# Optimization experiments

Hardware: AMD Instinct MI355X
Metric: run time of the kernel (lower is better)

## Reference

```python
import jax, jax.numpy as jnp
import numpy as np

B, L, HID = 32, 1, 3072
H, KV, D = 16, 8, 256
S = 2048
SCALE = D ** -0.5


def setup_inputs() -> dict:
    key = jax.random.key(0)
    ks = jax.random.split(key, 10)
    return {
        "hidden_states": jax.random.normal(ks[0], (B, L, HID), jnp.float32),
        "freqs_cos": jax.random.normal(ks[1], (B, L, D // 2), jnp.float32),
        "freqs_sin": jax.random.normal(ks[2], (B, L, D // 2), jnp.float32),
        "mask": jnp.zeros((B, 1, 1, S), jnp.float32),
        "cache_k": jax.random.normal(ks[3], (B, KV, S, D), jnp.float32),
        "cache_v": jax.random.normal(ks[4], (B, KV, S, D), jnp.float32),
        "wq": jax.random.normal(ks[5], (HID, H * D), jnp.float32) * 0.02,
        "wk": jax.random.normal(ks[6], (HID, KV * D), jnp.float32) * 0.02,
        "wv": jax.random.normal(ks[7], (HID, KV * D), jnp.float32) * 0.02,
        "wo": jax.random.normal(ks[8], (H * D, HID), jnp.float32) * 0.02,
        "pos": 2047,
    }


def _rope(x, cos, sin):
    # x: [B, L, nh, D]; cos/sin: [B, L, D/2]. Split-half complex rotation:
    # pairs are (x[..., i], x[..., i + D/2]), matching torch chunk+view_as_complex.
    half = x.shape[-1] // 2
    xr, xi = x[..., :half], x[..., half:]
    c = cos[:, :, None, :]
    s = sin[:, :, None, :]
    return jnp.concatenate([xr * c - xi * s, xr * s + xi * c], axis=-1)


def reference(hidden_states, freqs_cos, freqs_sin, mask, cache_k, cache_v,
              wq, wk, wv, wo, pos):
    G = H // KV  # queries per kv head
    xq = (hidden_states @ wq).reshape(B, L, H, D)
    xk = (hidden_states @ wk).reshape(B, L, KV, D)
    xv = (hidden_states @ wv).reshape(B, L, KV, D)

    xq = _rope(xq, freqs_cos, freqs_sin)
    xk = _rope(xk, freqs_cos, freqs_sin)

    # [B, heads, L, D]
    xq = xq.transpose(0, 2, 1, 3)
    xk = xk.transpose(0, 2, 1, 3)
    xv = xv.transpose(0, 2, 1, 3)

    # insert current step into the KV cache at static position `pos`
    cache_k = cache_k.at[:, :, pos:pos + L, :].set(xk)
    cache_v = cache_v.at[:, :, pos:pos + L, :].set(xv)

    # GQA attention over the full cache without materializing repeated KV
    q = xq.reshape(B, KV, G, L, D)
    scores = jnp.einsum('bkgqd,bksd->bkgqs', q, cache_k) * SCALE
    scores = scores + mask[:, :, None]  # [B,1,1,1,S] broadcast
    probs = jax.nn.softmax(scores, axis=-1)
    out = jnp.einsum('bkgqs,bksd->bkgqd', probs, cache_v)

    out = out.reshape(B, H, L, D).transpose(0, 2, 1, 3).reshape(B, L, H * D)
    return out @ wo
```

## Files before the change

### kernel.cpp

```cpp
#include <hip/hip_runtime.h>
#include <hip/hip_bf16.h>


#define SCALE_ 0.0625f

#define OFF_XQKV (8u*32u*8192u)
#define OFF_ATTN (OFF_XQKV + 32u*8192u)
#define OFF_PO   (OFF_ATTN + 32u*4096u)
#define OFF_ML   (1048576u)

__device__ inline void fma4(float4& a, float s, const float4& w) {
  a.x = fmaf(s, w.x, a.x); a.y = fmaf(s, w.y, a.y);
  a.z = fmaf(s, w.z, a.z); a.w = fmaf(s, w.w, a.w);
}
__device__ inline float dot4(const float4& a, const float4& b) {
  return a.x * b.x + a.y * b.y + a.z * b.z + a.w * b.w;
}
__device__ inline void scale_fma4(float4& a, float sc, float p, const float4& v) {
  a.x = fmaf(a.x, sc, p * v.x); a.y = fmaf(a.y, sc, p * v.y);
  a.z = fmaf(a.z, sc, p * v.z); a.w = fmaf(a.w, sc, p * v.w);
}

__global__ __launch_bounds__(512) void qkv_partial_kernel(
    const float* __restrict__ x, const float* __restrict__ wq,
    const float* __restrict__ wk, const float* __restrict__ wv,
    float* __restrict__ pqkv) {
  const int lane = threadIdx.x & 63;
  const int bg   = threadIdx.x >> 6;
  const int ctile = blockIdx.x & 31;
  const int kc    = blockIdx.x >> 5;
  const int n = ctile * 256 + lane * 4;

  const float* w; int stride, nn;
  if (n < 4096)      { w = wq; stride = 4096; nn = n; }
  else if (n < 6144) { w = wk; stride = 2048; nn = n - 4096; }
  else               { w = wv; stride = 2048; nn = n - 6144; }

  const float* wb = w + (size_t)(kc * 384) * stride + nn;
  const float* xb = x + (size_t)(bg * 4) * 3072 + kc * 384;

  float4 acc[4];
#pragma unroll
  for (int j = 0; j < 4; ++j) acc[j] = make_float4(0.f, 0.f, 0.f, 0.f);

  for (int k = 0; k < 384; k += 4) {
    float4 w0 = *(const float4*)(wb + (size_t)(k + 0) * stride);
    float4 w1 = *(const float4*)(wb + (size_t)(k + 1) * stride);
    float4 w2 = *(const float4*)(wb + (size_t)(k + 2) * stride);
    float4 w3 = *(const float4*)(wb + (size_t)(k + 3) * stride);
#pragma unroll
    for (int j = 0; j < 4; ++j) {
      float4 xv = *(const float4*)(xb + j * 3072 + k);
      fma4(acc[j], xv.x, w0);
      fma4(acc[j], xv.y, w1);
      fma4(acc[j], xv.z, w2);
      fma4(acc[j], xv.w, w3);
    }
  }
#pragma unroll
  for (int j = 0; j < 4; ++j) {
    *(float4*)(pqkv + ((size_t)kc * 32 + bg * 4 + j) * 8192 + n) = acc[j];
  }
}

__global__ __launch_bounds__(256) void reduce_rope_kernel(
    const float* __restrict__ pqkv, const float* __restrict__ fcos,
    const float* __restrict__ fsin, float* __restrict__ xqkv) {
  const int w = blockIdx.x * 256 + threadIdx.x;
  const int b = w / 5120;
  const int r = w - b * 5120;
  const float* pb = pqkv + (size_t)b * 8192;
  float* ob = xqkv + (size_t)b * 8192;

  if (r < 3072) {
    int n1, d;
    const bool isq = (r < 2048);
    if (isq) { int h = r >> 7; d = r & 127; n1 = h * 256 + d; }
    else     { int idx = r - 2048; int kvh = idx >> 7; d = idx & 127;
               n1 = 4096 + kvh * 256 + d; }
    const int n2 = n1 + 128;
    float xr = 0.f, xi = 0.f;
#pragma unroll
    for (int kc = 0; kc < 8; ++kc) {
      xr += pb[(size_t)kc * 262144 + n1];
      xi += pb[(size_t)kc * 262144 + n2];
    }
    const float c = fcos[b * 128 + d];
    const float s = fsin[b * 128 + d];
    float o1 = xr * c - xi * s;
    float o2 = xr * s + xi * c;
    if (isq) { o1 *= SCALE_; o2 *= SCALE_; }
    ob[n1] = o1;
    ob[n2] = o2;
  } else {
    const int nn = 6144 + (r - 3072);
    float v = 0.f;
#pragma unroll
    for (int kc = 0; kc < 8; ++kc) v += pb[(size_t)kc * 262144 + nn];
    ob[nn] = v;
  }
}

__global__ __launch_bounds__(256) void attn_chunk_kernel(
    const float* __restrict__ xqkv, const float* __restrict__ cache_k,
    const float* __restrict__ cache_v, const float* __restrict__ mask,
    const int* __restrict__ posp, float* __restrict__ opart,
    float* __restrict__ ml) {
  __shared__ float accbuf[8][512];
  __shared__ float mred[8][4];

  const int tid = threadIdx.x, lane = tid & 63, wv = tid >> 6;
  const int sub = lane & 31;
  const int stream = wv * 2 + (lane >> 5);
  const int c  = blockIdx.x & 7;
  const int kv = (blockIdx.x >> 3) & 7;
  const int b  = blockIdx.x >> 6;
  const int pos = posp[0];
  const int s0 = c * 256;
  const int dbase = sub * 8;

  const float* xb = xqkv + (size_t)b * 8192;
  const float* knew = xb + 4096 + kv * 256;
  const float* vnew = xb + 6144 + kv * 256;
  const size_t base = ((size_t)b * 8 + kv) * 2048 * 256;
  const float* kbase = cache_k + base;
  const float* vbase = cache_v + base;
  const float* mrow = mask + (size_t)b * 2048;

  const float4 qa0 = *(const float4*)(xb + (kv * 2 + 0) * 256 + dbase);
  const float4 qa1 = *(const float4*)(xb + (kv * 2 + 0) * 256 + dbase + 4);
  const float4 qb0 = *(const float4*)(xb + (kv * 2 + 1) * 256 + dbase);
  const float4 qb1 = *(const float4*)(xb + (kv * 2 + 1) * 256 + dbase + 4);

  float m0 = -3.4e38f, l0 = 0.f, m1 = -3.4e38f, l1 = 0.f;
  float4 a00 = make_float4(0.f, 0.f, 0.f, 0.f);
  float4 a01 = make_float4(0.f, 0.f, 0.f, 0.f);
  float4 a10 = make_float4(0.f, 0.f, 0.f, 0.f);
  float4 a11 = make_float4(0.f, 0.f, 0.f, 0.f);

  {
    const int s = s0 + stream;
    const float* kr = (s == pos) ? knew : (kbase + (size_t)s * 256);
    const float* vr = (s == pos) ? vnew : (vbase + (size_t)s * 256);
    float4 ka = *(const float4*)(kr + dbase);
    float4 kb = *(const float4*)(kr + dbase + 4);
    float4 va = *(const float4*)(vr + dbase);
    float4 vb = *(const float4*)(vr + dbase + 4);
    float mk = mrow[s];

    for (int i = 0; i < 32; ++i) {
      const float4 cka = ka, ckb = kb, cva = va, cvb = vb;
      const float cmk = mk;
      if (i < 31) {
        const int s2 = s0 + stream + 8 * (i + 1);
        const float* kr2 = (s2 == pos) ? knew : (kbase + (size_t)s2 * 256);
        const float* vr2 = (s2 == pos) ? vnew : (vbase + (size_t)s2 * 256);
        ka = *(const float4*)(kr2 + dbase);
        kb = *(const float4*)(kr2 + dbase + 4);
        va = *(const float4*)(vr2 + dbase);
        vb = *(const float4*)(vr2 + dbase + 4);
        mk = mrow[s2];
      }
      float d0 = dot4(qa0, cka) + dot4(qa1, ckb);
      float d1 = dot4(qb0, cka) + dot4(qb1, ckb);
#pragma unroll
      for (int off = 16; off > 0; off >>= 1) {
        d0 += __shfl_xor(d0, off);
        d1 += __shfl_xor(d1, off);
      }
      d0 += cmk; d1 += cmk;
      const float nm0 = fmaxf(m0, d0);
      const float al0 = __expf(m0 - nm0);
      const float p0  = __expf(d0 - nm0);
      m0 = nm0; l0 = fmaf(l0, al0, p0);
      scale_fma4(a00, al0, p0, cva);
      scale_fma4(a01, al0, p0, cvb);
      const float nm1 = fmaxf(m1, d1);
      const float al1 = __expf(m1 - nm1);
      const float p1  = __expf(d1 - nm1);
      m1 = nm1; l1 = fmaf(l1, al1, p1);
      scale_fma4(a10, al1, p1, cva);
      scale_fma4(a11, al1, p1, cvb);
    }
  }

  if (sub == 0) {
    mred[stream][0] = m0; mred[stream][1] = l0;
    mred[stream][2] = m1; mred[stream][3] = l1;
  }
  __syncthreads();
  float M0 = -3.4e38f, M1 = -3.4e38f;
#pragma unroll
  for (int t = 0; t < 8; ++t) {
    M0 = fmaxf(M0, mred[t][0]);
    M1 = fmaxf(M1, mred[t][2]);
  }
  const float sc0 = __expf(m0 - M0);
  const float sc1 = __expf(m1 - M1);
  float* ab = &accbuf[stream][0];
  ab[dbase + 0] = a00.x * sc0; ab[dbase + 1] = a00.y * sc0;
  ab[dbase + 2] = a00.z * sc0; ab[dbase + 3] = a00.w * sc0;
  ab[dbase + 4] = a01.x * sc0; ab[dbase + 5] = a01.y * sc0;
  ab[dbase + 6] = a01.z * sc0; ab[dbase + 7] = a01.w * sc0;
  ab[256 + dbase + 0] = a10.x * sc1; ab[256 + dbase + 1] = a10.y * sc1;
  ab[256 + dbase + 2] = a10.z * sc1; ab[256 + dbase + 3] = a10.w * sc1;
  ab[256 + dbase + 4] = a11.x * sc1; ab[256 + dbase + 5] = a11.y * sc1;
  ab[256 + dbase + 6] = a11.z * sc1; ab[256 + dbase + 7] = a11.w * sc1;
  __syncthreads();

  if (tid == 0) {
    float L0 = 0.f, L1 = 0.f;
#pragma unroll
    for (int t = 0; t < 8; ++t) {
      L0 = fmaf(mred[t][1], __expf(mred[t][0] - M0), L0);
      L1 = fmaf(mred[t][3], __expf(mred[t][2] - M1), L1);
    }
    float2* mlp = (float2*)ml;
    const int mlbase = (((b * 8 + kv) * 8) + c) * 2;
    mlp[mlbase + 0] = make_float2(M0, L0);
    mlp[mlbase + 1] = make_float2(M1, L1);
  }

  const size_t obase = (size_t)((b * 8 + kv) * 8 + c) * 512;
  for (int t = tid; t < 512; t += 256) {
    float sum = 0.f;
#pragma unroll
    for (int st = 0; st < 8; ++st) sum += accbuf[st][t];
    opart[obase + t] = sum;
  }
}

__global__ __launch_bounds__(256) void attn_combine_kernel(
    const float* __restrict__ opart, const float* __restrict__ ml,
    float* __restrict__ attn_out) {
  const int idx = blockIdx.x * 256 + threadIdx.x;
  const int d = idx & 255;
  const int g = (idx >> 8) & 1;
  const int kvb = idx >> 9;
  const float2* mlp = (const float2*)ml;

  float2 mls[8];
  float M = -3.4e38f;
#pragma unroll
  for (int c = 0; c < 8; ++c) {
    mls[c] = mlp[(kvb * 8 + c) * 2 + g];
    M = fmaxf(M, mls[c].x);
  }
  float L = 0.f, O = 0.f;
#pragma unroll
  for (int c = 0; c < 8; ++c) {
    const float w = __expf(mls[c].x - M);
    L = fmaf(mls[c].y, w, L);
    O = fmaf(opart[(size_t)(kvb * 8 + c) * 512 + g * 256 + d], w, O);
  }
  const int b = kvb >> 3, kv = kvb & 7;
  attn_out[(size_t)b * 4096 + (kv * 2 + g) * 256 + d] = O / L;
}

__global__ __launch_bounds__(512) void oproj_partial_kernel(
    const float* __restrict__ attn, const float* __restrict__ wo,
    float* __restrict__ po) {
  const int lane = threadIdx.x & 63;
  const int bg   = threadIdx.x >> 6;
  const int ctile = blockIdx.x % 12;
  const int kc    = blockIdx.x / 12;
  const int n = ctile * 256 + lane * 4;

  const float* wb = wo + (size_t)(kc * 256) * 3072 + n;
  const float* xb = attn + (size_t)(bg * 4) * 4096 + kc * 256;

  float4 acc[4];
#pragma unroll
  for (int j = 0; j < 4; ++j) acc[j] = make_float4(0.f, 0.f, 0.f, 0.f);

  for (int k = 0; k < 256; k += 4) {
    float4 w0 = *(const float4*)(wb + (size_t)(k + 0) * 3072);
    float4 w1 = *(const float4*)(wb + (size_t)(k + 1) * 3072);
    float4 w2 = *(const float4*)(wb + (size_t)(k + 2) * 3072);
    float4 w3 = *(const float4*)(wb + (size_t)(k + 3) * 3072);
#pragma unroll
    for (int j = 0; j < 4; ++j) {
      float4 xv = *(const float4*)(xb + j * 4096 + k);
      fma4(acc[j], xv.x, w0);
      fma4(acc[j], xv.y, w1);
      fma4(acc[j], xv.z, w2);
      fma4(acc[j], xv.w, w3);
    }
  }
#pragma unroll
  for (int j = 0; j < 4; ++j) {
    *(float4*)(po + ((size_t)kc * 32 + bg * 4 + j) * 3072 + n) = acc[j];
  }
}

__global__ __launch_bounds__(256) void finalize_kernel(
    const float* __restrict__ po, float* __restrict__ out) {
  const int i = blockIdx.x * 256 + threadIdx.x;
  const float4* p = (const float4*)po;
  float4 acc = make_float4(0.f, 0.f, 0.f, 0.f);
#pragma unroll
  for (int kc = 0; kc < 16; ++kc) {
    const float4 v = p[(size_t)kc * 24576 + i];
    acc.x += v.x; acc.y += v.y; acc.z += v.z; acc.w += v.w;
  }
  ((float4*)out)[i] = acc;
}

extern "C" void kernel_launch(void* const* d_in, const int* in_sizes, int n_in,
                              void* d_out, int out_size, void* d_ws, size_t ws_size,
                              hipStream_t stream) {
  (void)in_sizes; (void)n_in; (void)out_size; (void)ws_size;
  const float* x    = (const float*)d_in[0];
  const float* fcos = (const float*)d_in[1];
  const float* fsin = (const float*)d_in[2];
  const float* mask = (const float*)d_in[3];
  const float* ck   = (const float*)d_in[4];
  const float* cv   = (const float*)d_in[5];
  const float* wq   = (const float*)d_in[6];
  const float* wk   = (const float*)d_in[7];
  const float* wv   = (const float*)d_in[8];
  const float* wo   = (const float*)d_in[9];
  const int*   pos  = (const int*)d_in[10];

  float* ws    = (float*)d_ws;
  float* pqkv  = ws;
  float* opart = ws;
  float* ml    = ws + OFF_ML;
  float* xqkv  = ws + OFF_XQKV;
  float* attn  = ws + OFF_ATTN;
  float* po    = ws + OFF_PO;
  float* out   = (float*)d_out;

  qkv_partial_kernel<<<256, 512, 0, stream>>>(x, wq, wk, wv, pqkv);
  reduce_rope_kernel<<<640, 256, 0, stream>>>(pqkv, fcos, fsin, xqkv);
  attn_chunk_kernel<<<2048, 256, 0, stream>>>(xqkv, ck, cv, mask, pos, opart, ml);
  attn_combine_kernel<<<512, 256, 0, stream>>>(opart, ml, attn);
  oproj_partial_kernel<<<192, 512, 0, stream>>>(attn, wo, po);
  finalize_kernel<<<96, 256, 0, stream>>>(po, out);
}
```

Measured before the change: 329.7 us.

## Fuse attention combine into o-proj and deepen KV prefetch to two rows

The attention chunk loop now keeps two independent rows (A/B) of K/V in flight and issues the next loads early, so more memory requests are outstanding per thread to hide the latency of the KV-cache stream. The separate combine kernel is removed. Its split-softmax merge now runs inside the output projection kernel, which writes the normalised attention rows to shared memory before the GEMV. This saves one launch and a global round-trip of the attention output. The cost is that each o-proj block recomputes the combine for its own K-chunk, plus more registers in the attention loop.

```diff
diff --git a/kernel.cpp b/kernel.cpp
--- a/kernel.cpp
+++ b/kernel.cpp
@@ -138,49 +138,87 @@
   float4 a10 = make_float4(0.f, 0.f, 0.f, 0.f);
   float4 a11 = make_float4(0.f, 0.f, 0.f, 0.f);
 
-  {
-    const int s = s0 + stream;
-    const float* kr = (s == pos) ? knew : (kbase + (size_t)s * 256);
-    const float* vr = (s == pos) ? vnew : (vbase + (size_t)s * 256);
-    float4 ka = *(const float4*)(kr + dbase);
-    float4 kb = *(const float4*)(kr + dbase + 4);
-    float4 va = *(const float4*)(vr + dbase);
-    float4 vb = *(const float4*)(vr + dbase + 4);
-    float mk = mrow[s];
-
-    for (int i = 0; i < 32; ++i) {
-      const float4 cka = ka, ckb = kb, cva = va, cvb = vb;
-      const float cmk = mk;
-      if (i < 31) {
-        const int s2 = s0 + stream + 8 * (i + 1);
-        const float* kr2 = (s2 == pos) ? knew : (kbase + (size_t)s2 * 256);
-        const float* vr2 = (s2 == pos) ? vnew : (vbase + (size_t)s2 * 256);
-        ka = *(const float4*)(kr2 + dbase);
-        kb = *(const float4*)(kr2 + dbase + 4);
-        va = *(const float4*)(vr2 + dbase);
-        vb = *(const float4*)(vr2 + dbase + 4);
-        mk = mrow[s2];
-      }
-      float d0 = dot4(qa0, cka) + dot4(qa1, ckb);
-      float d1 = dot4(qb0, cka) + dot4(qb1, ckb);
+  int sA = s0 + stream;
+  int sB = sA + 8;
+  const float* krA = (sA == pos) ? knew : (kbase + (size_t)sA * 256);
+  const float* vrA = (sA == pos) ? vnew : (vbase + (size_t)sA * 256);
+  const float* krB = (sB == pos) ? knew : (kbase + (size_t)sB * 256);
+  const float* vrB = (sB == pos) ? vnew : (vbase + (size_t)sB * 256);
+  float4 kA0 = *(const float4*)(krA + dbase);
+  float4 kA1 = *(const float4*)(krA + dbase + 4);
+  float4 vA0 = *(const float4*)(vrA + dbase);
+  float4 vA1 = *(const float4*)(vrA + dbase + 4);
+  float mkA = mrow[sA];
+  float4 kB0 = *(const float4*)(krB + dbase);
+  float4 kB1 = *(const float4*)(krB + dbase + 4);
+  float4 vB0 = *(const float4*)(vrB + dbase);
+  float4 vB1 = *(const float4*)(vrB + dbase + 4);
+  float mkB = mrow[sB];
+
+  for (int i = 0; i < 32; i += 2) {
+    {
+      float d0 = dot4(qa0, kA0) + dot4(qa1, kA1);
+      float d1 = dot4(qb0, kA0) + dot4(qb1, kA1);
+      const int ipf = (i + 2 < 32) ? (i + 2) : 31;
+      const int sn = s0 + stream + 8 * ipf;
+      const float* krn = (sn == pos) ? knew : (kbase + (size_t)sn * 256);
+      const float* vrn = (sn == pos) ? vnew : (vbase + (size_t)sn * 256);
+      kA0 = *(const float4*)(krn + dbase);
+      kA1 = *(const float4*)(krn + dbase + 4);
+      const float mkn = mrow[sn];
 #pragma unroll
       for (int off = 16; off > 0; off >>= 1) {
         d0 += __shfl_xor(d0, off);
         d1 += __shfl_xor(d1, off);
       }
-      d0 += cmk; d1 += cmk;
+      d0 += mkA; d1 += mkA;
       const float nm0 = fmaxf(m0, d0);
       const float al0 = __expf(m0 - nm0);
       const float p0  = __expf(d0 - nm0);
       m0 = nm0; l0 = fmaf(l0, al0, p0);
-      scale_fma4(a00, al0, p0, cva);
-      scale_fma4(a01, al0, p0, cvb);
+      scale_fma4(a00, al0, p0, vA0);
+      scale_fma4(a01, al0, p0, vA1);
       const float nm1 = fmaxf(m1, d1);
       const float al1 = __expf(m1 - nm1);
       const float p1  = __expf(d1 - nm1);
       m1 = nm1; l1 = fmaf(l1, al1, p1);
-      scale_fma4(a10, al1, p1, cva);
-      scale_fma4(a11, al1, p1, cvb);
+      scale_fma4(a10, al1, p1, vA0);
+      scale_fma4(a11, al1, p1, vA1);
+      vA0 = *(const float4*)(vrn + dbase);
+      vA1 = *(const float4*)(vrn + dbase + 4);
+      mkA = mkn;
+    }
+    {
+      float d0 = dot4(qa0, kB0) + dot4(qa1, kB1);
+      float d1 = dot4(qb0, kB0) + dot4(qb1, kB1);
+      const int ipf = (i + 3 < 32) ? (i + 3) : 31;
+      const int sn = s0 + stream + 8 * ipf;
+      const float* krn = (sn == pos) ? knew : (kbase + (size_t)sn * 256);
+      const float* vrn = (sn == pos) ? vnew : (vbase + (size_t)sn * 256);
+      kB0 = *(const float4*)(krn + dbase);
+      kB1 = *(const float4*)(krn + dbase + 4);
+      const float mkn = mrow[sn];
+#pragma unroll
+      for (int off = 16; off > 0; off >>= 1) {
+        d0 += __shfl_xor(d0, off);
+        d1 += __shfl_xor(d1, off);
+      }
+      d0 += mkB; d1 += mkB;
+      const float nm0 = fmaxf(m0, d0);
+      const float al0 = __expf(m0 - nm0);
+      const float p0  = __expf(d0 - nm0);
+      m0 = nm0; l0 = fmaf(l0, al0, p0);
+      scale_fma4(a00, al0, p0, vB0);
+      scale_fma4(a01, al0, p0, vB1);
+      const float nm1 = fmaxf(m1, d1);
+      const float al1 = __expf(m1 - nm1);
+      const float p1  = __expf(d1 - nm1);
+      m1 = nm1; l1 = fmaf(l1, al1, p1);
+      scale_fma4(a10, al1, p1, vB0);
+      scale_fma4(a11, al1, p1, vB1);
+      vB0 = *(const float4*)(vrn + dbase);
+      vB1 = *(const float4*)(vrn + dbase + 4);
+      mkB = mkn;
     }
   }
 
@@ -230,44 +268,55 @@
   }
 }
 
-__global__ __launch_bounds__(256) void attn_combine_kernel(
+__global__ __launch_bounds__(512) void oproj_fused_kernel(
     const float* __restrict__ opart, const float* __restrict__ ml,
-    float* __restrict__ attn_out) {
-  const int idx = blockIdx.x * 256 + threadIdx.x;
-  const int d = idx & 255;
-  const int g = (idx >> 8) & 1;
-  const int kvb = idx >> 9;
-  const float2* mlp = (const float2*)ml;
-
-  float2 mls[8];
-  float M = -3.4e38f;
-#pragma unroll
-  for (int c = 0; c < 8; ++c) {
-    mls[c] = mlp[(kvb * 8 + c) * 2 + g];
-    M = fmaxf(M, mls[c].x);
-  }
-  float L = 0.f, O = 0.f;
-#pragma unroll
-  for (int c = 0; c < 8; ++c) {
-    const float w = __expf(mls[c].x - M);
-    L = fmaf(mls[c].y, w, L);
-    O = fmaf(opart[(size_t)(kvb * 8 + c) * 512 + g * 256 + d], w, O);
-  }
-  const int b = kvb >> 3, kv = kvb & 7;
-  attn_out[(size_t)b * 4096 + (kv * 2 + g) * 256 + d] = O / L;
-}
-
-__global__ __launch_bounds__(512) void oproj_partial_kernel(
-    const float* __restrict__ attn, const float* __restrict__ wo,
-    float* __restrict__ po) {
-  const int lane = threadIdx.x & 63;
-  const int bg   = threadIdx.x >> 6;
+    const float* __restrict__ wo, float* __restrict__ po) {
+  __shared__ float xs[32][256];
+
+  const int t = threadIdx.x;
   const int ctile = blockIdx.x % 12;
   const int kc    = blockIdx.x / 12;
+  const int kvh = kc >> 1, g = kc & 1;
+
+  {
+    const int b = t >> 4;
+    const int d0 = (t & 15) * 16;
+    const int kvb = b * 8 + kvh;
+    const float2* mlp = (const float2*)ml;
+    float2 mls[8];
+    float M = -3.4e38f;
+#pragma unroll
+    for (int c = 0; c < 8; ++c) {
+      mls[c] = mlp[(kvb * 8 + c) * 2 + g];
+      M = fmaxf(M, mls[c].x);
+    }
+    float L = 0.f;
+    float4 O[4];
+#pragma unroll
+    for (int q = 0; q < 4; ++q) O[q] = make_float4(0.f, 0.f, 0.f, 0.f);
+#pragma unroll
+    for (int c = 0; c < 8; ++c) {
+      const float wc = __expf(mls[c].x - M);
+      L = fmaf(mls[c].y, wc, L);
+      const float4* src =
+          (const float4*)(opart + (size_t)(kvb * 8 + c) * 512 + g * 256 + d0);
+      fma4(O[0], wc, src[0]); fma4(O[1], wc, src[1]);
+      fma4(O[2], wc, src[2]); fma4(O[3], wc, src[3]);
+    }
+    const float invL = 1.f / L;
+    float4* dst = (float4*)(&xs[b][d0]);
+#pragma unroll
+    for (int q = 0; q < 4; ++q) {
+      dst[q] = make_float4(O[q].x * invL, O[q].y * invL,
+                           O[q].z * invL, O[q].w * invL);
+    }
+  }
+  __syncthreads();
+
+  const int lane = t & 63;
+  const int bg   = t >> 6;
   const int n = ctile * 256 + lane * 4;
-
   const float* wb = wo + (size_t)(kc * 256) * 3072 + n;
-  const float* xb = attn + (size_t)(bg * 4) * 4096 + kc * 256;
 
   float4 acc[4];
 #pragma unroll
@@ -280,11 +329,11 @@
     float4 w3 = *(const float4*)(wb + (size_t)(k + 3) * 3072);
 #pragma unroll
     for (int j = 0; j < 4; ++j) {
-      float4 xv = *(const float4*)(xb + j * 4096 + k);
-      fma4(acc[j], xv.x, w0);
-      fma4(acc[j], xv.y, w1);
-      fma4(acc[j], xv.z, w2);
-      fma4(acc[j], xv.w, w3);
+      const float* xr = &xs[bg * 4 + j][k];
+      fma4(acc[j], xr[0], w0);
+      fma4(acc[j], xr[1], w1);
+      fma4(acc[j], xr[2], w2);
+      fma4(acc[j], xr[3], w3);
     }
   }
 #pragma unroll
@@ -327,14 +376,12 @@
   float* opart = ws;
   float* ml    = ws + OFF_ML;
   float* xqkv  = ws + OFF_XQKV;
-  float* attn  = ws + OFF_ATTN;
   float* po    = ws + OFF_PO;
   float* out   = (float*)d_out;
 
   qkv_partial_kernel<<<256, 512, 0, stream>>>(x, wq, wk, wv, pqkv);
   reduce_rope_kernel<<<640, 256, 0, stream>>>(pqkv, fcos, fsin, xqkv);
   attn_chunk_kernel<<<2048, 256, 0, stream>>>(xqkv, ck, cv, mask, pos, opart, ml);
-  attn_combine_kernel<<<512, 256, 0, stream>>>(opart, ml, attn);
-  oproj_partial_kernel<<<192, 512, 0, stream>>>(attn, wo, po);
+  oproj_fused_kernel<<<192, 512, 0, stream>>>(opart, ml, wo, po);
   finalize_kernel<<<96, 256, 0, stream>>>(po, out);
 }
```

Result: no change. 324.5 us (-1.6%).
